# Kernel optimization log

Hardware: AMD Instinct MI355X
Metric: run time of the kernel (lower is better)

Reference implementation:

```python
import jax, jax.numpy as jnp
import numpy as np

D_IN = 1024
D_OUT = 1024
NUM_HEADS = 16
HEAD_DIM = D_OUT // NUM_HEADS


def setup_inputs() -> dict:
    key = jax.random.key(0)
    ks = jax.random.split(key, 6)
    scale = 0.02
    x = jax.random.normal(ks[0], (4, 2048, D_IN), dtype=jnp.float32)
    Wq = jax.random.normal(ks[1], (D_IN, D_OUT), dtype=jnp.float32) * scale
    Wk = jax.random.normal(ks[2], (D_IN, D_OUT), dtype=jnp.float32) * scale
    Wv = jax.random.normal(ks[3], (D_IN, D_OUT), dtype=jnp.float32) * scale
    Wo = jax.random.normal(ks[4], (D_OUT, D_OUT), dtype=jnp.float32) * scale
    bo = jax.random.normal(ks[5], (D_OUT,), dtype=jnp.float32) * scale
    return {"x": x, "Wq": Wq, "Wk": Wk, "Wv": Wv, "Wo": Wo, "bo": bo}


def reference(x, Wq, Wk, Wv, Wo, bo):
    b, n, _ = x.shape
    # QKV projections -> [b, h, n, hd]
    def split_heads(t):
        return t.reshape(b, n, NUM_HEADS, HEAD_DIM).transpose(0, 2, 1, 3)
    q = split_heads(x @ Wq)
    k = split_heads(x @ Wk)
    v = split_heads(x @ Wv)
    # scaled causal attention scores [b, h, n, n]
    scores = jnp.einsum('bhqd,bhkd->bhqk', q, k) / jnp.sqrt(jnp.float32(HEAD_DIM))
    causal = jnp.tril(jnp.ones((n, n), dtype=bool))
    scores = jnp.where(causal, scores, -jnp.inf)
    attn = jax.nn.softmax(scores, axis=-1)
    # dropout p=0.0 -> identity
    ctx = jnp.einsum('bhqk,bhkd->bhqd', attn, v)  # [b, h, n, hd]
    ctx = ctx.transpose(0, 2, 1, 3).reshape(b, n, D_OUT)
    return ctx @ Wo + bo
```

## Files before the change

### kernel.cpp

```cpp
#include <hip/hip_runtime.h>
#include <hip/hip_bf16.h>

typedef __bf16 bf16;
typedef __attribute__((ext_vector_type(8))) __bf16 bf16x8;
typedef __attribute__((ext_vector_type(4))) __bf16 bf16x4;
typedef __attribute__((ext_vector_type(4))) float floatx4;

#define DM 1024
#define NH 16
#define HD 64
#define SEQ 2048
#define BATCH 4
#define MTOT (BATCH * SEQ)

#if __has_builtin(__builtin_amdgcn_exp2f)
#define EXP2(x) __builtin_amdgcn_exp2f(x)
#else
#define EXP2(x) exp2f(x)
#endif

#define GLDS(g, l) \
  __builtin_amdgcn_global_load_lds((const __attribute__((address_space(1))) void*)(g), \
                                   (__attribute__((address_space(3))) void*)(l), 16, 0, 0)

__global__ void prep(const float* __restrict__ x,
                     const float* __restrict__ Wq, const float* __restrict__ Wk,
                     const float* __restrict__ Wv, const float* __restrict__ Wo,
                     bf16* __restrict__ xb, bf16* __restrict__ Wqkvt, bf16* __restrict__ Wot) {
  __shared__ float tile[32][33];
  int bid = blockIdx.x, tid = threadIdx.x;
  if (bid < 8192) {
    int i = bid * 256 + tid;
    float4 v = ((const float4*)x)[i];
    bf16x4 o;
    o[0] = (bf16)v.x; o[1] = (bf16)v.y; o[2] = (bf16)v.z; o[3] = (bf16)v.w;
    ((bf16x4*)xb)[i] = o;
    return;
  }
  int b2 = bid - 8192;
  int z = b2 >> 10, t = b2 & 1023;
  const float* W;
  bf16* Wt;
  if (z == 0) { W = Wq; Wt = Wqkvt; }
  else if (z == 1) { W = Wk; Wt = Wqkvt + (size_t)DM * DM; }
  else if (z == 2) { W = Wv; Wt = Wqkvt + (size_t)2 * DM * DM; }
  else { W = Wo; Wt = Wot; }
  int n0 = (t & 31) * 32, k0 = (t >> 5) * 32;
  int tx = tid & 31, ty = tid >> 5;
#pragma unroll
  for (int j = 0; j < 32; j += 8)
    tile[ty + j][tx] = W[(size_t)(k0 + ty + j) * DM + n0 + tx];
  __syncthreads();
#pragma unroll
  for (int j = 0; j < 32; j += 8)
    Wt[(size_t)(n0 + ty + j) * DM + k0 + tx] = (bf16)tile[tx][ty + j];
}

#define BK 64

__global__ __launch_bounds__(256, 3) void gemm_qkv(const bf16* __restrict__ A,
                                                   const bf16* __restrict__ Bt,
                                                   bf16* __restrict__ Qb,
                                                   bf16* __restrict__ Kb,
                                                   bf16* __restrict__ Vt) {
  __shared__ __align__(16) bf16 Alds[128 * BK];
  __shared__ __align__(16) bf16 Blds[128 * BK];
  const int K = 1024;
  int m0 = blockIdx.x * 128;
  int n0 = blockIdx.y * 128;
  int tid = threadIdx.x;
  int wave = tid >> 6, lane = tid & 63;
  int wm = (wave & 1) * 64, wn = (wave >> 1) * 64;
  int lm = lane & 15, quad = lane >> 4;
  int lm7 = lm & 7;

  int cbase = wave * 64 + lane;
  const bf16* gA[4];
  const bf16* gB[4];
  bf16 *lA[4], *lB[4];
#pragma unroll
  for (int seg = 0; seg < 4; ++seg) {
    int c = seg * 256 + cbase;
    int row = c >> 3;
    int col8 = (c & 7) ^ (row & 7);
    gA[seg] = A + (size_t)(m0 + row) * K + col8 * 8;
    gB[seg] = Bt + (size_t)(n0 + row) * K + col8 * 8;
    lA[seg] = Alds + c * 8;
    lB[seg] = Blds + c * 8;
  }

  floatx4 acc[4][4] = {};
  for (int kt = 0; kt < K; kt += BK) {
    __syncthreads();
#pragma unroll
    for (int seg = 0; seg < 4; ++seg) {
      GLDS(gA[seg] + kt, lA[seg]);
      GLDS(gB[seg] + kt, lB[seg]);
    }
    __syncthreads();
#pragma unroll
    for (int ks = 0; ks < 2; ++ks) {
      int xk = (ks * 4 + quad) ^ lm7;
      bf16x8 af[4], bfr[4];
#pragma unroll
      for (int t = 0; t < 4; ++t) {
        af[t] = *(const bf16x8*)(Alds + (wm + t * 16 + lm) * BK + xk * 8);
        bfr[t] = *(const bf16x8*)(Blds + (wn + t * 16 + lm) * BK + xk * 8);
      }
#pragma unroll
      for (int i = 0; i < 4; ++i)
#pragma unroll
        for (int j = 0; j < 4; ++j)
          acc[i][j] = __builtin_amdgcn_mfma_f32_16x16x32_bf16(af[i], bfr[j], acc[i][j], 0, 0, 0);
    }
  }

  int proj = n0 >> 10;
  if (proj == 2) {
#pragma unroll
    for (int i = 0; i < 4; ++i) {
      int Rb = m0 + wm + i * 16 + quad * 4;
      int b = Rb >> 11, nb = Rb & 2047;
#pragma unroll
      for (int j = 0; j < 4; ++j) {
        int cc = (n0 + wn + j * 16 + lm) & 1023;
        int h = cc >> 6, d = cc & 63;
        bf16x4 ov;
#pragma unroll
        for (int r = 0; r < 4; ++r) ov[r] = (bf16)acc[i][j][r];
        *(bf16x4*)(Vt + ((size_t)(b * NH + h) * HD + d) * SEQ + nb) = ov;
      }
    }
  } else {
    bf16* P = proj ? Kb : Qb;
#pragma unroll
    for (int i = 0; i < 4; ++i) {
#pragma unroll
      for (int j = 0; j < 4; ++j) {
        int cc = (n0 + wn + j * 16 + lm) & 1023;
        int h = cc >> 6, d = cc & 63;
#pragma unroll
        for (int r = 0; r < 4; ++r) {
          int R = m0 + wm + i * 16 + quad * 4 + r;
          int b = R >> 11, n = R & 2047;
          P[((size_t)(b * NH + h) * SEQ + n) * HD + d] = (bf16)acc[i][j][r];
        }
      }
    }
  }
}

__global__ __launch_bounds__(256, 3) void gemm_out(const bf16* __restrict__ A,
                                                   const bf16* __restrict__ Bt,
                                                   const float* __restrict__ bias,
                                                   float* __restrict__ out) {
  __shared__ __align__(16) bf16 Alds[128 * BK];
  __shared__ __align__(16) bf16 Blds[128 * BK];
  const int K = 1024;
  int m0 = blockIdx.x * 128;
  int n0 = blockIdx.y * 128;
  int tid = threadIdx.x;
  int wave = tid >> 6, lane = tid & 63;
  int wm = (wave & 1) * 64, wn = (wave >> 1) * 64;
  int lm = lane & 15, quad = lane >> 4;
  int lm7 = lm & 7;

  int cbase = wave * 64 + lane;
  const bf16* gA[4];
  const bf16* gB[4];
  bf16 *lA[4], *lB[4];
#pragma unroll
  for (int seg = 0; seg < 4; ++seg) {
    int c = seg * 256 + cbase;
    int row = c >> 3;
    int col8 = (c & 7) ^ (row & 7);
    gA[seg] = A + (size_t)(m0 + row) * K + col8 * 8;
    gB[seg] = Bt + (size_t)(n0 + row) * K + col8 * 8;
    lA[seg] = Alds + c * 8;
    lB[seg] = Blds + c * 8;
  }

  floatx4 acc[4][4] = {};
  for (int kt = 0; kt < K; kt += BK) {
    __syncthreads();
#pragma unroll
    for (int seg = 0; seg < 4; ++seg) {
      GLDS(gA[seg] + kt, lA[seg]);
      GLDS(gB[seg] + kt, lB[seg]);
    }
    __syncthreads();
#pragma unroll
    for (int ks = 0; ks < 2; ++ks) {
      int xk = (ks * 4 + quad) ^ lm7;
      bf16x8 af[4], bfr[4];
#pragma unroll
      for (int t = 0; t < 4; ++t) {
        af[t] = *(const bf16x8*)(Alds + (wm + t * 16 + lm) * BK + xk * 8);
        bfr[t] = *(const bf16x8*)(Blds + (wn + t * 16 + lm) * BK + xk * 8);
      }
#pragma unroll
      for (int i = 0; i < 4; ++i)
#pragma unroll
        for (int j = 0; j < 4; ++j)
          acc[i][j] = __builtin_amdgcn_mfma_f32_16x16x32_bf16(af[i], bfr[j], acc[i][j], 0, 0, 0);
    }
  }
#pragma unroll
  for (int i = 0; i < 4; ++i)
#pragma unroll
    for (int j = 0; j < 4; ++j)
#pragma unroll
      for (int r = 0; r < 4; ++r) {
        int R = m0 + wm + i * 16 + quad * 4 + r;
        int C = n0 + wn + j * 16 + lm;
        out[(size_t)R * DM + C] = acc[i][j][r] + bias[C];
      }
}

__global__ __launch_bounds__(512, 2) void attn(const bf16* __restrict__ Qb,
                                               const bf16* __restrict__ Kb,
                                               const bf16* __restrict__ Vt,
                                               bf16* __restrict__ ctx) {
  __shared__ __align__(16) bf16 KV[4][4096];
  int blk = blockIdx.x;
  int xcd = blk & 7;
  int idx = blk >> 3;
  int bh = (idx & 7) * 8 + xcd;
  int pr = idx >> 3;
  int tid = threadIdx.x, wave = tid >> 6, lane = tid & 63;
  int qg = wave & 3, par = wave >> 2;
  int lm = lane & 15, quad = lane >> 4;
  int lm7 = lm & 7;
  const bf16* Qp = Qb + (size_t)bh * SEQ * HD;
  const bf16* Kp = Kb + (size_t)bh * SEQ * HD;
  const bf16* Vp = Vt + (size_t)bh * HD * SEQ;
  int b = bh >> 4, h = bh & 15;
  const float QSCALE = 0.125f * 1.4426950408889634f;

  int c = tid;
  int r = c >> 3, l = (c & 7) ^ (r & 7);
  const bf16* Kg = Kp + (size_t)r * HD + l * 8;
  const bf16* Vg = Vp + (size_t)r * SEQ + (l >> 2) * 32 + (l & 3) * 4;

  const bf16* Kl = KV[par];
  const bf16* Vl = KV[2 + par];

  bf16x8 ones;
#pragma unroll
  for (int j = 0; j < 8; ++j) ones[j] = (lm == 0) ? (bf16)1.0f : (bf16)0.0f;

  int xk0 = (quad ^ lm7) * 8;
  int xk1 = ((4 + quad) ^ lm7) * 8;

  float* cbuf = (float*)&KV[0][0];
  int cb = qg * 1088 + lane;

#pragma unroll 1
  for (int half = 0; half < 2; ++half) {
    int qt = half ? pr : 15 - pr;
    int q0 = qt * 128;
    int rowbase = q0 + qg * 32;
    int ns = qt + 1;

    bf16x8 qfA[2], qfB[2];
#pragma unroll
    for (int ks2 = 0; ks2 < 2; ++ks2) {
      bf16x8 qa = *(const bf16x8*)(Qp + (size_t)(rowbase + lm) * HD + ks2 * 32 + quad * 8);
      bf16x8 qb = *(const bf16x8*)(Qp + (size_t)(rowbase + 16 + lm) * HD + ks2 * 32 + quad * 8);
#pragma unroll
      for (int j = 0; j < 8; ++j) {
        qa[j] = (bf16)((float)qa[j] * QSCALE);
        qb[j] = (bf16)((float)qb[j] * QSCALE);
      }
      qfA[ks2] = qa;
      qfB[ks2] = qb;
    }

    floatx4 accA[4] = {}, accB[4] = {};
    floatx4 aclA = {}, aclB = {};

    if (half) __syncthreads();

    bf16x8 kr0 = *(const bf16x8*)(Kg);
    bf16x8 kr1 = *(const bf16x8*)(Kg + (size_t)64 * HD);
    bf16x4 v0a = *(const bf16x4*)(Vg),      v0b = *(const bf16x4*)(Vg + 16);
    bf16x4 v1a = *(const bf16x4*)(Vg + 64), v1b = *(const bf16x4*)(Vg + 80);
    *(bf16x8*)(KV[0] + c * 8) = kr0;
    *(bf16x8*)(KV[1] + c * 8) = kr1;
    *(bf16x4*)(KV[2] + c * 8) = v0a; *(bf16x4*)(KV[2] + c * 8 + 4) = v0b;
    *(bf16x4*)(KV[3] + c * 8) = v1a; *(bf16x4*)(KV[3] + c * 8 + 4) = v1b;

#pragma unroll 1
    for (int s = 0; s < ns; ++s) {
      __syncthreads();
      if (s + 1 < ns) {
        int kt = (2 * s + 2) * 64;
        kr0 = *(const bf16x8*)(Kg + (size_t)kt * HD);
        kr1 = *(const bf16x8*)(Kg + (size_t)(kt + 64) * HD);
        v0a = *(const bf16x4*)(Vg + kt);      v0b = *(const bf16x4*)(Vg + kt + 16);
        v1a = *(const bf16x4*)(Vg + kt + 64); v1b = *(const bf16x4*)(Vg + kt + 80);
      }
      int kv0 = (2 * s + par) * 64;

      if (kv0 <= rowbase + 31) {
        floatx4 stA[4] = {}, stB[4] = {};
#pragma unroll
        for (int mt = 0; mt < 4; ++mt) {
          const bf16* kr = Kl + (mt * 16 + lm) * 64;
          bf16x8 kf0 = *(const bf16x8*)(kr + xk0);
          bf16x8 kf1 = *(const bf16x8*)(kr + xk1);
          stA[mt] = __builtin_amdgcn_mfma_f32_16x16x32_bf16(kf0, qfA[0], stA[mt], 0, 0, 0);
          stA[mt] = __builtin_amdgcn_mfma_f32_16x16x32_bf16(kf1, qfA[1], stA[mt], 0, 0, 0);
          stB[mt] = __builtin_amdgcn_mfma_f32_16x16x32_bf16(kf0, qfB[0], stB[mt], 0, 0, 0);
          stB[mt] = __builtin_amdgcn_mfma_f32_16x16x32_bf16(kf1, qfB[1], stB[mt], 0, 0, 0);
        }

        bf16x8 pfA2[2], pfB2[2];
        if (kv0 + 63 <= rowbase) {
#pragma unroll
          for (int mt = 0; mt < 4; ++mt)
#pragma unroll
            for (int rr = 0; rr < 4; ++rr) {
              pfA2[mt >> 1][(mt & 1) * 4 + rr] = (bf16)EXP2(stA[mt][rr]);
              pfB2[mt >> 1][(mt & 1) * 4 + rr] = (bf16)EXP2(stB[mt][rr]);
            }
        } else {
          int qrelA = rowbase - kv0 + lm;
          int qrelB = qrelA + 16;
#pragma unroll
          for (int mt = 0; mt < 4; ++mt)
#pragma unroll
            for (int rr = 0; rr < 4; ++rr) {
              int kvrel = mt * 16 + quad * 4 + rr;
              float pa = EXP2(stA[mt][rr]);
              float pbv = EXP2(stB[mt][rr]);
              if (kvrel > qrelA) pa = 0.f;
              if (kvrel > qrelB) pbv = 0.f;
              pfA2[mt >> 1][(mt & 1) * 4 + rr] = (bf16)pa;
              pfB2[mt >> 1][(mt & 1) * 4 + rr] = (bf16)pbv;
            }
        }

#pragma unroll
        for (int ks = 0; ks < 2; ++ks) {
          int xv = ks ? xk1 : xk0;
          aclA = __builtin_amdgcn_mfma_f32_16x16x32_bf16(ones, pfA2[ks], aclA, 0, 0, 0);
          aclB = __builtin_amdgcn_mfma_f32_16x16x32_bf16(ones, pfB2[ks], aclB, 0, 0, 0);
#pragma unroll
          for (int db = 0; db < 4; ++db) {
            bf16x8 vf = *(const bf16x8*)(Vl + (db * 16 + lm) * 64 + xv);
            accA[db] = __builtin_amdgcn_mfma_f32_16x16x32_bf16(vf, pfA2[ks], accA[db], 0, 0, 0);
            accB[db] = __builtin_amdgcn_mfma_f32_16x16x32_bf16(vf, pfB2[ks], accB[db], 0, 0, 0);
          }
        }
      }

      if (s + 1 < ns) {
        __syncthreads();
        *(bf16x8*)(KV[0] + c * 8) = kr0;
        *(bf16x8*)(KV[1] + c * 8) = kr1;
        *(bf16x4*)(KV[2] + c * 8) = v0a; *(bf16x4*)(KV[2] + c * 8 + 4) = v0b;
        *(bf16x4*)(KV[3] + c * 8) = v1a; *(bf16x4*)(KV[3] + c * 8 + 4) = v1b;
      }
    }

    __syncthreads();
    if (par) {
#pragma unroll
      for (int db = 0; db < 4; ++db)
#pragma unroll
        for (int rr = 0; rr < 4; ++rr)
          cbuf[cb + (db * 4 + rr) * 64] = accA[db][rr];
      cbuf[cb + 1024] = aclA[0];
    }
    __syncthreads();
    float aA = aclA[0], aB = aclB[0];
    if (!par) {
#pragma unroll
      for (int db = 0; db < 4; ++db)
#pragma unroll
        for (int rr = 0; rr < 4; ++rr)
          accA[db][rr] += cbuf[cb + (db * 4 + rr) * 64];
      aA += cbuf[cb + 1024];
    }
    __syncthreads();
    if (par) {
#pragma unroll
      for (int db = 0; db < 4; ++db)
#pragma unroll
        for (int rr = 0; rr < 4; ++rr)
          cbuf[cb + (db * 4 + rr) * 64] = accB[db][rr];
      cbuf[cb + 1024] = aclB[0];
    }
    __syncthreads();
    if (!par) {
#pragma unroll
      for (int db = 0; db < 4; ++db)
#pragma unroll
        for (int rr = 0; rr < 4; ++rr)
          accB[db][rr] += cbuf[cb + (db * 4 + rr) * 64];
      aB += cbuf[cb + 1024];

      float linvA = 1.0f / __shfl(aA, lm, 64);
      float linvB = 1.0f / __shfl(aB, lm, 64);

      bf16* crowA = ctx + ((size_t)b * SEQ + rowbase + lm) * DM + h * 64;
      bf16* crowB = crowA + (size_t)16 * DM;
#pragma unroll
      for (int db = 0; db < 4; ++db) {
        bf16x4 oa, ob;
#pragma unroll
        for (int rr = 0; rr < 4; ++rr) {
          oa[rr] = (bf16)(accA[db][rr] * linvA);
          ob[rr] = (bf16)(accB[db][rr] * linvB);
        }
        *(bf16x4*)(crowA + db * 16 + quad * 4) = oa;
        *(bf16x4*)(crowB + db * 16 + quad * 4) = ob;
      }
    }
  }
}

extern "C" void kernel_launch(void* const* d_in, const int* in_sizes, int n_in,
                              void* d_out, int out_size, void* d_ws, size_t ws_size,
                              hipStream_t stream) {
  const float* x = (const float*)d_in[0];
  const float* Wq = (const float*)d_in[1];
  const float* Wk = (const float*)d_in[2];
  const float* Wv = (const float*)d_in[3];
  const float* Wo = (const float*)d_in[4];
  const float* bo = (const float*)d_in[5];
  float* out = (float*)d_out;

  bf16* ws = (bf16*)d_ws;
  bf16* xb = ws;
  bf16* Wqkvt = xb + (size_t)MTOT * DM;
  bf16* Wot = Wqkvt + (size_t)3 * DM * DM;
  bf16* Qb = Wot + (size_t)DM * DM;
  bf16* Kb = Qb + (size_t)BATCH * NH * SEQ * HD;
  bf16* Vtb = Kb + (size_t)BATCH * NH * SEQ * HD;
  bf16* ctx = xb;

  prep<<<8192 + 4096, 256, 0, stream>>>(x, Wq, Wk, Wv, Wo, xb, Wqkvt, Wot);
  gemm_qkv<<<dim3(MTOT / 128, 3 * DM / 128), 256, 0, stream>>>(xb, Wqkvt, Qb, Kb, Vtb);
  attn<<<512, 512, 0, stream>>>(Qb, Kb, Vtb, ctx);
  gemm_out<<<dim3(MTOT / 128, DM / 128), 256, 0, stream>>>(ctx, Wot, bo, out);
}
```

Before: 223.0 us.

## Double-buffer K/V tiles in LDS and merge partial-sum reduction passes

```diff
diff --git a/kernel.cpp b/kernel.cpp
--- a/kernel.cpp
+++ b/kernel.cpp
@@ -221,7 +221,7 @@
                                                const bf16* __restrict__ Kb,
                                                const bf16* __restrict__ Vt,
                                                bf16* __restrict__ ctx) {
-  __shared__ __align__(16) bf16 KV[4][4096];
+  __shared__ __align__(16) bf16 KV[32768];
   int blk = blockIdx.x;
   int xcd = blk & 7;
   int idx = blk >> 3;
@@ -242,8 +242,8 @@
   const bf16* Kg = Kp + (size_t)r * HD + l * 8;
   const bf16* Vg = Vp + (size_t)r * SEQ + (l >> 2) * 32 + (l & 3) * 4;
 
-  const bf16* Kl = KV[par];
-  const bf16* Vl = KV[2 + par];
+  int kread = par * 4096;
+  int vread = 8192 + par * 4096;
 
   bf16x8 ones;
 #pragma unroll
@@ -252,8 +252,8 @@
   int xk0 = (quad ^ lm7) * 8;
   int xk1 = ((4 + quad) ^ lm7) * 8;
 
-  float* cbuf = (float*)&KV[0][0];
-  int cb = qg * 1088 + lane;
+  float* cbuf = (float*)&KV[0];
+  int cb = qg * 2176 + lane;
 
 #pragma unroll 1
   for (int half = 0; half < 2; ++half) {
@@ -285,15 +285,18 @@
     bf16x8 kr1 = *(const bf16x8*)(Kg + (size_t)64 * HD);
     bf16x4 v0a = *(const bf16x4*)(Vg),      v0b = *(const bf16x4*)(Vg + 16);
     bf16x4 v1a = *(const bf16x4*)(Vg + 64), v1b = *(const bf16x4*)(Vg + 80);
-    *(bf16x8*)(KV[0] + c * 8) = kr0;
-    *(bf16x8*)(KV[1] + c * 8) = kr1;
-    *(bf16x4*)(KV[2] + c * 8) = v0a; *(bf16x4*)(KV[2] + c * 8 + 4) = v0b;
-    *(bf16x4*)(KV[3] + c * 8) = v1a; *(bf16x4*)(KV[3] + c * 8 + 4) = v1b;
+    *(bf16x8*)(KV + c * 8) = kr0;
+    *(bf16x8*)(KV + 4096 + c * 8) = kr1;
+    *(bf16x4*)(KV + 8192 + c * 8) = v0a;  *(bf16x4*)(KV + 8192 + c * 8 + 4) = v0b;
+    *(bf16x4*)(KV + 12288 + c * 8) = v1a; *(bf16x4*)(KV + 12288 + c * 8 + 4) = v1b;
 
 #pragma unroll 1
     for (int s = 0; s < ns; ++s) {
       __syncthreads();
-      if (s + 1 < ns) {
+      int bofs = (s & 1) << 14;
+      int nofs = bofs ^ 16384;
+      bool pf = (s + 1 < ns);
+      if (pf) {
         int kt = (2 * s + 2) * 64;
         kr0 = *(const bf16x8*)(Kg + (size_t)kt * HD);
         kr1 = *(const bf16x8*)(Kg + (size_t)(kt + 64) * HD);
@@ -303,6 +306,8 @@
       int kv0 = (2 * s + par) * 64;
 
       if (kv0 <= rowbase + 31) {
+        const bf16* Kl = KV + bofs + kread;
+        const bf16* Vl = KV + bofs + vread;
         floatx4 stA[4] = {}, stB[4] = {};
 #pragma unroll
         for (int mt = 0; mt < 4; ++mt) {
@@ -355,12 +360,11 @@
         }
       }
 
-      if (s + 1 < ns) {
-        __syncthreads();
-        *(bf16x8*)(KV[0] + c * 8) = kr0;
-        *(bf16x8*)(KV[1] + c * 8) = kr1;
-        *(bf16x4*)(KV[2] + c * 8) = v0a; *(bf16x4*)(KV[2] + c * 8 + 4) = v0b;
-        *(bf16x4*)(KV[3] + c * 8) = v1a; *(bf16x4*)(KV[3] + c * 8 + 4) = v1b;
+      if (pf) {
+        *(bf16x8*)(KV + nofs + c * 8) = kr0;
+        *(bf16x8*)(KV + nofs + 4096 + c * 8) = kr1;
+        *(bf16x4*)(KV + nofs + 8192 + c * 8) = v0a;  *(bf16x4*)(KV + nofs + 8192 + c * 8 + 4) = v0b;
+        *(bf16x4*)(KV + nofs + 12288 + c * 8) = v1a; *(bf16x4*)(KV + nofs + 12288 + c * 8 + 4) = v1b;
       }
     }
 
@@ -369,37 +373,24 @@
 #pragma unroll
       for (int db = 0; db < 4; ++db)
 #pragma unroll
-        for (int rr = 0; rr < 4; ++rr)
+        for (int rr = 0; rr < 4; ++rr) {
           cbuf[cb + (db * 4 + rr) * 64] = accA[db][rr];
-      cbuf[cb + 1024] = aclA[0];
-    }
-    __syncthreads();
-    float aA = aclA[0], aB = aclB[0];
+          cbuf[cb + (17 + db * 4 + rr) * 64] = accB[db][rr];
+        }
+      cbuf[cb + 16 * 64] = aclA[0];
+      cbuf[cb + 33 * 64] = aclB[0];
+    }
+    __syncthreads();
     if (!par) {
+      float aA = aclA[0] + cbuf[cb + 16 * 64];
+      float aB = aclB[0] + cbuf[cb + 33 * 64];
 #pragma unroll
       for (int db = 0; db < 4; ++db)
 #pragma unroll
-        for (int rr = 0; rr < 4; ++rr)
+        for (int rr = 0; rr < 4; ++rr) {
           accA[db][rr] += cbuf[cb + (db * 4 + rr) * 64];
-      aA += cbuf[cb + 1024];
-    }
-    __syncthreads();
-    if (par) {
-#pragma unroll
-      for (int db = 0; db < 4; ++db)
-#pragma unroll
-        for (int rr = 0; rr < 4; ++rr)
-          cbuf[cb + (db * 4 + rr) * 64] = accB[db][rr];
-      cbuf[cb + 1024] = aclB[0];
-    }
-    __syncthreads();
-    if (!par) {
-#pragma unroll
-      for (int db = 0; db < 4; ++db)
-#pragma unroll
-        for (int rr = 0; rr < 4; ++rr)
-          accB[db][rr] += cbuf[cb + (db * 4 + rr) * 64];
-      aB += cbuf[cb + 1024];
+          accB[db][rr] += cbuf[cb + (17 + db * 4 + rr) * 64];
+        }
 
       float linvA = 1.0f / __shfl(aA, lm, 64);
       float linvB = 1.0f / __shfl(aB, lm, 64);
```

Measured after the change: 220.5 us (median of 3 runs). No clear change (-1.1%).
